# Optimization experiments

Hardware: AMD Instinct MI355X
Metric: run time of the kernel (lower is better)

The kernel has to match this reference:

```python
import jax, jax.numpy as jnp
import numpy as np

K_N = 20          # neighbors (init kwarg k_n)
EPS = 1e-5        # BN / InstanceNorm eps (torch default)


def _conv1x1(x, w, b):
    # x: [B,C,N,K], w: [O,C], b: [O]
    return jnp.einsum('bcnk,oc->bonk', x, w) + b[None, :, None, None]


def _bn(x, g, b):
    # training-mode BatchNorm2d: stats over (B,N,K)
    mean = x.mean(axis=(0, 2, 3), keepdims=True)
    var = x.var(axis=(0, 2, 3), keepdims=True)
    return (x - mean) * jax.lax.rsqrt(var + EPS) * g[None, :, None, None] + b[None, :, None, None]


def _inorm(x):
    # InstanceNorm2d (affine=False): stats over (N,K) per (b,c)
    mean = x.mean(axis=(2, 3), keepdims=True)
    var = x.var(axis=(2, 3), keepdims=True)
    return (x - mean) * jax.lax.rsqrt(var + EPS)


def _knn(x, k):
    # x: [B,C,N] -> idx [B,N,k] of nearest neighbors (excluding self)
    sq = jnp.sum(x * x, axis=1)                                   # [B,N]
    neg_d = 2.0 * jnp.einsum('bcn,bcm->bnm', x, x) - sq[:, :, None] - sq[:, None, :]
    _, idx = jax.lax.top_k(neg_d, k + 1)
    return idx[:, :, 1:]


def _res_block(x, w1, b1, g1, be1, w2, b2, g2, be2):
    # pre=False: residual branch is identity
    out = jax.nn.relu(_bn(_inorm(_conv1x1(x, w1, b1)), g1, be1))
    out = _bn(_inorm(_conv1x1(out, w2, b2)), g2, be2)
    return jax.nn.relu(out + x)


def _forward(data, conv0_w, conv0_b, bn0_g, bn0_b, lin_w, lin_b,
             res_w1, res_b1, res_g1, res_be1, res_w2, res_b2, res_g2, res_be2):
    B, C, N = data.shape
    # graph_feature: degree feature from normalized affinity matrix
    nrm = jnp.linalg.norm(data, axis=1, keepdims=True) + 1e-5
    o = data / nrm
    A = jnp.einsum('bcn,bcm->bnm', o, o)                          # [B,N,N]
    D = (jnp.sum(A, axis=1, keepdims=True) - 1.0) / N             # [B,1,N] (subtract eye diag)
    feat = jnp.concatenate([data, jax.nn.relu(jnp.tanh(D))], axis=1)  # [B,129,N]

    idx = _knn(feat, K_N)                                         # [B,N,k]
    xt = jnp.transpose(feat, (0, 2, 1))                           # [B,N,129]
    gathered = jax.vmap(lambda xb, ib: xb[ib])(xt, idx)           # [B,N,k,129]
    center = xt[:, :, None, :]
    edge = jnp.concatenate([jnp.broadcast_to(center, gathered.shape),
                            center - gathered], axis=3)           # [B,N,k,258]
    edge = jnp.transpose(edge, (0, 3, 1, 2))                      # [B,258,N,k]

    out = jax.nn.relu(_bn(_conv1x1(edge, conv0_w, conv0_b), bn0_g, bn0_b))
    out = jnp.max(out, axis=3, keepdims=True)                     # max_pool2d (1,k) -> [B,128,N,1]
    for i in range(4):
        out = _res_block(out, res_w1[i], res_b1[i], res_g1[i], res_be1[i],
                         res_w2[i], res_b2[i], res_g2[i], res_be2[i])
    logit = _conv1x1(out, lin_w, lin_b)                           # [B,1,N,1]
    return logit.reshape(logit.shape[0], -1)                      # [B,N]


def setup_inputs() -> dict:
    B, C, N = 8, 128, 2048
    key = jax.random.key(0)
    ks = jax.random.split(key, 10)
    s = 0.05
    return {
        'data': jax.random.normal(ks[0], (B, C, N), dtype=jnp.float32),
        'x': jax.random.normal(ks[1], (B, C, N), dtype=jnp.float32),  # unused by module
        'conv0_w': jax.random.normal(ks[2], (128, 258), dtype=jnp.float32) * s,
        'conv0_b': jnp.zeros((128,), dtype=jnp.float32),
        'bn0_g': jnp.ones((128,), dtype=jnp.float32),
        'bn0_b': jnp.zeros((128,), dtype=jnp.float32),
        'lin_w': jax.random.normal(ks[3], (1, 128), dtype=jnp.float32) * s,
        'lin_b': jnp.zeros((1,), dtype=jnp.float32),
        'res_w1': jax.random.normal(ks[4], (4, 128, 128), dtype=jnp.float32) * s,
        'res_b1': jnp.zeros((4, 128), dtype=jnp.float32),
        'res_g1': jnp.ones((4, 128), dtype=jnp.float32),
        'res_be1': jnp.zeros((4, 128), dtype=jnp.float32),
        'res_w2': jax.random.normal(ks[5], (4, 128, 128), dtype=jnp.float32) * s,
        'res_b2': jnp.zeros((4, 128), dtype=jnp.float32),
        'res_g2': jnp.ones((4, 128), dtype=jnp.float32),
        'res_be2': jnp.zeros((4, 128), dtype=jnp.float32),
    }


def reference(data, x, conv0_w, conv0_b, bn0_g, bn0_b, lin_w, lin_b,
              res_w1, res_b1, res_g1, res_be1, res_w2, res_b2, res_g2, res_be2):
    # x is accepted but unused, matching the torch module
    return _forward(data, conv0_w, conv0_b, bn0_g, bn0_b, lin_w, lin_b,
                    res_w1, res_b1, res_g1, res_be1, res_w2, res_b2, res_g2, res_be2)
```

## Files before the change

kernel.cpp:

```cpp
#include <hip/hip_runtime.h>
#include <math.h>
#include <float.h>

#define NB 8
#define NC 128
#define NN 2048
#define KNN 20
#define EPSV 1e-5f

#define S_OFF      0
#define BN0S_OFF   1024
#define RESST_OFF  1280
#define ZERO_CNT   17664
#define NRM_OFF    17664
#define SQN_OFF    34048
#define F1_OFF     50432
#define WCAT_OFF   66816
#define WCOL_OFF   99584
#define F128_OFF   99840
#define PQ_OFF     2463232
#define X_OFF      6657536
#define SLOT_SZ    2097152
#define IDX_OFF    12948992
#define G_OFF      13276672
#define XB_OFF     46831104
#define WS_FLOATS  48928256
#define MMN_OFF    (X_OFF + SLOT_SZ)
#define MMX_OFF    (X_OFF + 2 * SLOT_SZ)

__launch_bounds__(256)
__global__ void k1_fused(const float* __restrict__ data, float* __restrict__ ws) {
    int b = blockIdx.y;
    int n0 = blockIdx.x * 64;
    int tid = threadIdx.x;
    __shared__ float tile[128][65];
    __shared__ float red[4][64];
    __shared__ float Linv[64];
    int g = tid >> 6, nn = tid & 63;
    const float* dp = data + (size_t)b * NC * NN + n0 + nn;
    float sq = 0.f;
    for (int c = g; c < 128; c += 4) {
        float v = dp[(size_t)c * NN];
        tile[c][nn] = v;
        sq = fmaf(v, v, sq);
    }
    red[g][nn] = sq;
    __syncthreads();
    if (tid < 64) {
        float s = red[0][tid] + red[1][tid] + red[2][tid] + red[3][tid];
        ws[NRM_OFF + b * NN + n0 + tid] = s;
        Linv[tid] = 1.f / (sqrtf(s) + 1e-5f);
    }
    __syncthreads();
    if (tid < 128) {
        float s = 0.f;
#pragma unroll 8
        for (int j = 0; j < 64; ++j) s = fmaf(tile[tid][j], Linv[j], s);
        atomicAdd(&ws[S_OFF + b * NC + tid], s);
    }
}

__launch_bounds__(256)
__global__ void k2_feat(const float* __restrict__ data, float* __restrict__ ws) {
    int b = blockIdx.y;
    int n0 = blockIdx.x * 64;
    int tid = threadIdx.x;
    __shared__ float Sb[NC];
    __shared__ float fT[64][129];
    __shared__ float redD[4][64];
    if (tid < NC) Sb[tid] = ws[S_OFF + b * NC + tid];
    __syncthreads();
    int nn = tid & 63, cg = tid >> 6;
    float dotp = 0.f;
    const float* dp = data + (size_t)b * NC * NN + n0 + nn;
    for (int c = cg; c < NC; c += 4) {
        float v = dp[(size_t)c * NN];
        fT[nn][c] = v;
        dotp = fmaf(Sb[c], v, dotp);
    }
    redD[cg][nn] = dotp;
    __syncthreads();
    if (tid < 64) {
        float dt = redD[0][tid] + redD[1][tid] + redD[2][tid] + redD[3][tid];
        float nrmsq = ws[NRM_OFF + b * NN + n0 + tid];
        float nrm = sqrtf(nrmsq) + 1e-5f;
        float D = (dt / nrm - 1.f) * (1.f / (float)NN);
        float f1 = tanhf(D); if (f1 < 0.f) f1 = 0.f;
        ws[F1_OFF + b * NN + n0 + tid] = f1;
        ws[SQN_OFF + b * NN + n0 + tid] = nrmsq + f1 * f1;
    }
    __syncthreads();
    float* out = ws + F128_OFF + (size_t)(b * NN + n0) * 128;
    for (int i = tid; i < 64 * 128; i += 256) out[i] = fT[i >> 7][i & 127];
}

__launch_bounds__(256)
__global__ void k4_wcat(const float* __restrict__ w, float* __restrict__ ws) {
    int i = blockIdx.x * 256 + threadIdx.x;
    if (i < 32768) {
        int o = i >> 7, c = i & 127;
        float v = (o < 128) ? w[o * 258 + c] + w[o * 258 + 129 + c]
                            : w[(o - 128) * 258 + 129 + c];
        ws[WCAT_OFF + i] = v;
    } else if (i < 33024) {
        int o = i - 32768;
        float v = (o < 128) ? w[o * 258 + 128] + w[o * 258 + 257]
                            : w[(o - 128) * 258 + 257];
        ws[WCOL_OFF + o] = v;
    }
}

__launch_bounds__(256)
__global__ void k3_gram(float* __restrict__ ws) {
    __shared__ __align__(16) float As[8][64];
    __shared__ __align__(16) float Bs[8][128];
    int tid = threadIdx.x;
    int b = blockIdx.z;
    int p = blockIdx.x >> 1, half = blockIdx.x & 1;
    int a = 0, rem = 16;
    while (p >= rem) { p -= rem; ++a; --rem; }
    int bq = a + p;
    int n0 = a * 128 + half * 64, m0 = bq * 128;
    const float* F = ws + F128_OFF + (size_t)b * NN * 128;
    float acc[4][8];
#pragma unroll
    for (int i = 0; i < 4; ++i)
#pragma unroll
        for (int j = 0; j < 8; ++j) acc[i][j] = 0.f;
    int rr = tid >> 1, cq = tid & 1;
    int ar = (tid & 127) >> 1, acq = tid & 1;
    int tx = tid & 15, ty = tid >> 4;
    for (int kc = 0; kc < 128; kc += 8) {
        float4 bv = *(const float4*)&F[(size_t)(m0 + rr) * 128 + kc + cq * 4];
        float4 av;
        if (tid < 128) av = *(const float4*)&F[(size_t)(n0 + ar) * 128 + kc + acq * 4];
        __syncthreads();
        Bs[cq*4+0][rr] = bv.x; Bs[cq*4+1][rr] = bv.y; Bs[cq*4+2][rr] = bv.z; Bs[cq*4+3][rr] = bv.w;
        if (tid < 128) {
            As[acq*4+0][ar] = av.x; As[acq*4+1][ar] = av.y;
            As[acq*4+2][ar] = av.z; As[acq*4+3][ar] = av.w;
        }
        __syncthreads();
#pragma unroll
        for (int kk = 0; kk < 8; ++kk) {
            float aa[4], bb[8];
            *(float4*)&aa[0] = *(const float4*)&As[kk][ty * 4];
            *(float4*)&bb[0] = *(const float4*)&Bs[kk][tx * 4];
            *(float4*)&bb[4] = *(const float4*)&Bs[kk][64 + tx * 4];
#pragma unroll
            for (int i = 0; i < 4; ++i)
#pragma unroll
                for (int j = 0; j < 8; ++j) acc[i][j] = fmaf(aa[i], bb[j], acc[i][j]);
        }
    }
    const float* F1 = ws + F1_OFF + b * NN;
    const float* SQ = ws + SQN_OFF + b * NN;
    float sqv[8], f1m[8], sqn[4], f1nv[4];
#pragma unroll
    for (int j = 0; j < 4; ++j) {
        sqv[j]     = SQ[m0 + tx * 4 + j];
        sqv[4 + j] = SQ[m0 + 64 + tx * 4 + j];
        f1m[j]     = F1[m0 + tx * 4 + j];
        f1m[4 + j] = F1[m0 + 64 + tx * 4 + j];
    }
#pragma unroll
    for (int i = 0; i < 4; ++i) {
        int n = n0 + ty * 4 + i;
        sqn[i]  = SQ[n];
        f1nv[i] = F1[n];
    }
    float* G = ws + G_OFF + (size_t)b * NN * NN;
#pragma unroll
    for (int i = 0; i < 4; ++i) {
        int row = n0 + ty * 4 + i;
        float f1n = f1nv[i];
        float4 o1, o2;
        o1.x = 2.f*fmaf(f1n, f1m[0], acc[i][0]) - sqv[0];
        o1.y = 2.f*fmaf(f1n, f1m[1], acc[i][1]) - sqv[1];
        o1.z = 2.f*fmaf(f1n, f1m[2], acc[i][2]) - sqv[2];
        o1.w = 2.f*fmaf(f1n, f1m[3], acc[i][3]) - sqv[3];
        o2.x = 2.f*fmaf(f1n, f1m[4], acc[i][4]) - sqv[4];
        o2.y = 2.f*fmaf(f1n, f1m[5], acc[i][5]) - sqv[5];
        o2.z = 2.f*fmaf(f1n, f1m[6], acc[i][6]) - sqv[6];
        o2.w = 2.f*fmaf(f1n, f1m[7], acc[i][7]) - sqv[7];
        *(float4*)&G[(size_t)row * NN + m0 + tx * 4]      = o1;
        *(float4*)&G[(size_t)row * NN + m0 + 64 + tx * 4] = o2;
    }
    if (a != bq) {
#pragma unroll
        for (int j = 0; j < 8; ++j) {
            int cl = (j < 4) ? (tx * 4 + j) : (64 + tx * 4 + (j - 4));
            size_t grow = (size_t)(m0 + cl) * NN + n0 + ty * 4;
            float f1mj = f1m[j];
            float4 t0;
            t0.x = 2.f*fmaf(f1nv[0], f1mj, acc[0][j]) - sqn[0];
            t0.y = 2.f*fmaf(f1nv[1], f1mj, acc[1][j]) - sqn[1];
            t0.z = 2.f*fmaf(f1nv[2], f1mj, acc[2][j]) - sqn[2];
            t0.w = 2.f*fmaf(f1nv[3], f1mj, acc[3][j]) - sqn[3];
            *(float4*)&G[grow] = t0;
        }
    }
}

__launch_bounds__(256)
__global__ void ksel(float* __restrict__ ws) {
    int wid = threadIdx.x >> 6, lane = threadIdx.x & 63;
    int r = blockIdx.x * 4 + wid;
    const float* row = ws + G_OFF + (size_t)r * NN;
    float v[32];
#pragma unroll
    for (int i = 0; i < 8; ++i)
        *(float4*)&v[i * 4] = *(const float4*)&row[lane * 32 + i * 4];
    float b1v = -FLT_MAX, b2v = -FLT_MAX;
    int b1i = 0, b2i = 0;
#pragma unroll
    for (int i = 0; i < 32; ++i) {
        float x = v[i];
        if (x > b1v)      { b2v = b1v; b2i = b1i; b1v = x; b1i = i; }
        else if (x > b2v) { b2v = x; b2i = i; }
    }
    unsigned int mask = 0u;
    bool has2 = true;
    int* out = (int*)(ws + IDX_OFF) + (size_t)r * KNN;
    for (int k = 0; k < 21; ++k) {
        float M = b1v;
#pragma unroll
        for (int off = 1; off < 64; off <<= 1) M = fmaxf(M, __shfl_xor(M, off));
        unsigned long long tied = __ballot(b1v == M);
        int mm;
        if (__popcll(tied) > 1) {
            int cand = (b1v == M) ? ((lane << 5) | b1i) : 0x7FFFFFFF;
#pragma unroll
            for (int off = 1; off < 64; off <<= 1) {
                int oc = __shfl_xor(cand, off);
                cand = oc < cand ? oc : cand;
            }
            mm = cand;
        } else {
            int l = __ffsll(tied) - 1;
            mm = (l << 5) | __shfl(b1i, l);
        }
        if (k > 0 && lane == 0) out[k - 1] = mm;
        if (lane == (mm >> 5)) {
            mask |= 1u << b1i;
            if (has2) { b1v = b2v; b1i = b2i; has2 = false; }
            else {
                b1v = -FLT_MAX; b2v = -FLT_MAX; b1i = 0; b2i = 0;
#pragma unroll
                for (int i = 0; i < 32; ++i) {
                    float x = (mask & (1u << i)) ? -FLT_MAX : v[i];
                    if (x > b1v)      { b2v = b1v; b2i = b1i; b1v = x; b1i = i; }
                    else if (x > b2v) { b2v = x; b2i = i; }
                }
                has2 = true;
            }
        }
    }
}

__launch_bounds__(256)
__global__ void k5_pq(float* __restrict__ ws) {
    __shared__ __align__(16) float As[16][64];
    __shared__ __align__(16) float Bs[16][64];
    int tid = threadIdx.x;
    int m0 = blockIdx.x * 64, o0 = blockIdx.y * 64;
    int rr = tid >> 2, cq = tid & 3;
    int tx = tid & 15, ty = tid >> 4;
    float acc[4][4];
#pragma unroll
    for (int i = 0; i < 4; ++i)
#pragma unroll
        for (int j = 0; j < 4; ++j) acc[i][j] = 0.f;
    const float* F  = ws + F128_OFF;
    const float* Wc = ws + WCAT_OFF;
    for (int kc = 0; kc < 128; kc += 16) {
        float4 av = *(const float4*)&F [(size_t)(m0 + rr) * 128 + kc + cq * 4];
        float4 bv = *(const float4*)&Wc[(size_t)(o0 + rr) * 128 + kc + cq * 4];
        __syncthreads();
        As[cq*4+0][rr]=av.x; As[cq*4+1][rr]=av.y; As[cq*4+2][rr]=av.z; As[cq*4+3][rr]=av.w;
        Bs[cq*4+0][rr]=bv.x; Bs[cq*4+1][rr]=bv.y; Bs[cq*4+2][rr]=bv.z; Bs[cq*4+3][rr]=bv.w;
        __syncthreads();
#pragma unroll
        for (int kk = 0; kk < 16; ++kk) {
            float a[4], bb[4];
            *(float4*)&a[0]  = *(const float4*)&As[kk][ty * 4];
            *(float4*)&bb[0] = *(const float4*)&Bs[kk][tx * 4];
#pragma unroll
            for (int i = 0; i < 4; ++i)
#pragma unroll
                for (int j = 0; j < 4; ++j) acc[i][j] = fmaf(a[i], bb[j], acc[i][j]);
        }
    }
    float wc[4], f1v[4];
#pragma unroll
    for (int j = 0; j < 4; ++j) {
        wc[j]  = ws[WCOL_OFF + o0 + tx * 4 + j];
        f1v[j] = ws[F1_OFF + m0 + ty * 4 + j];
    }
#pragma unroll
    for (int i = 0; i < 4; ++i) {
        float4 o;
        o.x = fmaf(f1v[i], wc[0], acc[i][0]);
        o.y = fmaf(f1v[i], wc[1], acc[i][1]);
        o.z = fmaf(f1v[i], wc[2], acc[i][2]);
        o.w = fmaf(f1v[i], wc[3], acc[i][3]);
        *(float4*)&ws[PQ_OFF + (size_t)(m0 + ty * 4 + i) * 256 + o0 + tx * 4] = o;
    }
}

__launch_bounds__(256)
__global__ void k6_bn0stats(float* __restrict__ ws) {
    int tid = threadIdx.x;
    int o = tid & 127, h = tid >> 7;
    int m0 = blockIdx.x * 16;
    const float* PQ = ws + PQ_OFF;
    const int* idx = (const int*)(ws + IDX_OFF);
    float* MMn = ws + MMN_OFF;
    float* MMx = ws + MMX_OFF;
    __shared__ float red[2][128];
    float s = 0.f, q = 0.f;
    for (int p = h; p < 16; p += 2) {
        int m = m0 + p;
        int bb = m >> 11;
        float pv = PQ[(size_t)m * 256 + o];
        const int* ip = idx + (size_t)m * KNN;
        float mn = FLT_MAX, mx = -FLT_MAX;
        for (int k = 0; k < KNN; ++k) {
            int j = ip[k];
            float val = pv - PQ[(size_t)(bb * NN + j) * 256 + 128 + o];
            s += val; q += val * val;
            mn = fminf(mn, val); mx = fmaxf(mx, val);
        }
        MMn[(size_t)m * NC + o] = mn;
        MMx[(size_t)m * NC + o] = mx;
    }
    red[h][o] = s; __syncthreads();
    if (tid < 128) atomicAdd(&ws[BN0S_OFF + tid], red[0][tid] + red[1][tid]);
    __syncthreads();
    red[h][o] = q; __syncthreads();
    if (tid < 128) atomicAdd(&ws[BN0S_OFF + 128 + tid], red[0][tid] + red[1][tid]);
}

__launch_bounds__(256)
__global__ void k8_apply(float* __restrict__ ws, const float* __restrict__ g,
                         const float* __restrict__ be) {
    int e = blockIdx.x * 256 + threadIdx.x;
    int fi = e * 4;
    int o = fi & 127;
    const float cnt = 1.f / (float)(NB * NN * KNN);
    float4 sum4 = *(const float4*)&ws[BN0S_OFF + o];
    float4 ssq4 = *(const float4*)&ws[BN0S_OFF + 128 + o];
    float4 g4   = *(const float4*)&g[o];
    float4 be4  = *(const float4*)&be[o];
    float4 mn = *(const float4*)&ws[MMN_OFF + fi];
    float4 mx = *(const float4*)&ws[MMX_OFF + fi];
    float4 r;
#define BN0_DO(comp) { \
    float m_ = sum4.comp * cnt; \
    float v_ = ssq4.comp * cnt - m_ * m_; if (v_ < 0.f) v_ = 0.f; \
    float sc_ = g4.comp * rsqrtf(v_ + EPSV); \
    float sh_ = be4.comp - m_ * sc_; \
    r.comp = fmaxf(fmaf(sc_ > 0.f ? mx.comp : mn.comp, sc_, sh_), 0.f); }
    BN0_DO(x) BN0_DO(y) BN0_DO(z) BN0_DO(w)
#undef BN0_DO
    *(float4*)&ws[X_OFF + fi] = r;
}

__launch_bounds__(256)
__global__ void k9f_conv(const float* __restrict__ x, const float* __restrict__ w,
                         float* __restrict__ y, float* __restrict__ stats,
                         const float* __restrict__ statsIn,
                         const float* __restrict__ g, const float* __restrict__ be,
                         const float* __restrict__ xin, float* __restrict__ xw) {
    __shared__ __align__(16) float As[16][64];
    __shared__ __align__(16) float Bs[16][64];
    __shared__ float red[16][64];
    __shared__ float vvv[8][128];
    __shared__ float scs[128], shs[128];
    int tid = threadIdx.x;
    int m0 = blockIdx.x * 64, o0 = blockIdx.y * 64;
    int bA = m0 >> 11;
    if (statsIn) {
        for (int e = tid; e < 1024; e += 256) {
            float sum = statsIn[e], ssq = statsIn[1024 + e];
            float m_ = sum * (1.f / (float)NN);
            float v_ = ssq * (1.f / (float)NN) - m_ * m_; if (v_ < 0.f) v_ = 0.f;
            vvv[e >> 7][e & 127] = v_ / (v_ + EPSV);
        }
        __syncthreads();
        if (tid < 128) {
            float a = 0.f;
#pragma unroll
            for (int b2 = 0; b2 < NB; ++b2) a += vvv[b2][tid];
            float rsbn = rsqrtf(a * (1.f / (float)NB) + EPSV);
            float sum = statsIn[bA * 128 + tid], ssq = statsIn[1024 + bA * 128 + tid];
            float m_ = sum * (1.f / (float)NN);
            float v_ = ssq * (1.f / (float)NN) - m_ * m_; if (v_ < 0.f) v_ = 0.f;
            float sc_ = rsqrtf(v_ + EPSV) * rsbn * g[tid];
            scs[tid] = sc_;
            shs[tid] = be[tid] - m_ * sc_;
        }
        __syncthreads();
    }
    int rr = tid >> 2, cq = tid & 3;
    int tx = tid & 15, ty = tid >> 4;
    float acc[4][4];
#pragma unroll
    for (int i = 0; i < 4; ++i)
#pragma unroll
        for (int j = 0; j < 4; ++j) acc[i][j] = 0.f;
    for (int kc = 0; kc < NC; kc += 16) {
        float4 av = *(const float4*)&x[(size_t)(m0 + rr) * NC + kc + cq * 4];
        if (statsIn) {
            int c = kc + cq * 4;
            av.x = fmaf(av.x, scs[c],     shs[c]);
            av.y = fmaf(av.y, scs[c + 1], shs[c + 1]);
            av.z = fmaf(av.z, scs[c + 2], shs[c + 2]);
            av.w = fmaf(av.w, scs[c + 3], shs[c + 3]);
            if (xin) {
                float4 xv = *(const float4*)&xin[(size_t)(m0 + rr) * NC + kc + cq * 4];
                av.x += xv.x; av.y += xv.y; av.z += xv.z; av.w += xv.w;
            }
            av.x = fmaxf(av.x, 0.f); av.y = fmaxf(av.y, 0.f);
            av.z = fmaxf(av.z, 0.f); av.w = fmaxf(av.w, 0.f);
            if (xw && blockIdx.y == 0)
                *(float4*)&xw[(size_t)(m0 + rr) * NC + kc + cq * 4] = av;
        }
        float4 bv = *(const float4*)&w[(size_t)(o0 + rr) * NC + kc + cq * 4];
        __syncthreads();
        As[cq*4+0][rr]=av.x; As[cq*4+1][rr]=av.y; As[cq*4+2][rr]=av.z; As[cq*4+3][rr]=av.w;
        Bs[cq*4+0][rr]=bv.x; Bs[cq*4+1][rr]=bv.y; Bs[cq*4+2][rr]=bv.z; Bs[cq*4+3][rr]=bv.w;
        __syncthreads();
#pragma unroll
        for (int kk = 0; kk < 16; ++kk) {
            float a[4], bb[4];
            *(float4*)&a[0]  = *(const float4*)&As[kk][ty * 4];
            *(float4*)&bb[0] = *(const float4*)&Bs[kk][tx * 4];
#pragma unroll
            for (int i = 0; i < 4; ++i)
#pragma unroll
                for (int j = 0; j < 4; ++j) acc[i][j] = fmaf(a[i], bb[j], acc[i][j]);
        }
    }
#pragma unroll
    for (int i = 0; i < 4; ++i) {
        float4 o;
        o.x = acc[i][0]; o.y = acc[i][1]; o.z = acc[i][2]; o.w = acc[i][3];
        *(float4*)&y[(size_t)(m0 + ty * 4 + i) * NC + o0 + tx * 4] = o;
    }
    float s[4], q[4];
#pragma unroll
    for (int j = 0; j < 4; ++j) {
        s[j] = acc[0][j] + acc[1][j] + acc[2][j] + acc[3][j];
        q[j] = acc[0][j]*acc[0][j] + acc[1][j]*acc[1][j] + acc[2][j]*acc[2][j] + acc[3][j]*acc[3][j];
    }
    *(float4*)&red[ty][tx * 4] = make_float4(s[0], s[1], s[2], s[3]);
    __syncthreads();
    if (tid < 64) {
        float t = 0.f;
#pragma unroll
        for (int g2 = 0; g2 < 16; ++g2) t += red[g2][tid];
        atomicAdd(&stats[bA * NC + o0 + tid], t);
    }
    __syncthreads();
    *(float4*)&red[ty][tx * 4] = make_float4(q[0], q[1], q[2], q[3]);
    __syncthreads();
    if (tid < 64) {
        float t = 0.f;
#pragma unroll
        for (int g2 = 0; g2 < 16; ++g2) t += red[g2][tid];
        atomicAdd(&stats[1024 + bA * NC + o0 + tid], t);
    }
}

__launch_bounds__(256)
__global__ void k12_logit(const float* __restrict__ y2, const float* __restrict__ xin,
                          const float* __restrict__ statsIn,
                          const float* __restrict__ g, const float* __restrict__ be,
                          const float* __restrict__ lw, const float* __restrict__ lb,
                          float* __restrict__ out) {
    __shared__ float wsh[128];
    __shared__ float vvv[8][128];
    __shared__ float scs[128], shs[128];
    int tid = threadIdx.x;
    int b = (blockIdx.x * 256) >> 11;
    if (tid < 128) wsh[tid] = lw[tid];
    for (int e = tid; e < 1024; e += 256) {
        float sum = statsIn[e], ssq = statsIn[1024 + e];
        float m_ = sum * (1.f / (float)NN);
        float v_ = ssq * (1.f / (float)NN) - m_ * m_; if (v_ < 0.f) v_ = 0.f;
        vvv[e >> 7][e & 127] = v_ / (v_ + EPSV);
    }
    __syncthreads();
    if (tid < 128) {
        float a = 0.f;
#pragma unroll
        for (int b2 = 0; b2 < NB; ++b2) a += vvv[b2][tid];
        float rsbn = rsqrtf(a * (1.f / (float)NB) + EPSV);
        float sum = statsIn[b * 128 + tid], ssq = statsIn[1024 + b * 128 + tid];
        float m_ = sum * (1.f / (float)NN);
        float v_ = ssq * (1.f / (float)NN) - m_ * m_; if (v_ < 0.f) v_ = 0.f;
        float sc_ = rsqrtf(v_ + EPSV) * rsbn * g[tid];
        scs[tid] = sc_;
        shs[tid] = be[tid] - m_ * sc_;
    }
    __syncthreads();
    int m = blockIdx.x * 256 + tid;
    const float* yp = y2 + (size_t)m * NC;
    const float* xp = xin + (size_t)m * NC;
    float acc = lb[0];
    for (int c = 0; c < NC; c += 4) {
        float4 yv = *(const float4*)&yp[c];
        float4 xv = *(const float4*)&xp[c];
        float v0 = fmaxf(fmaf(yv.x, scs[c],     shs[c])     + xv.x, 0.f);
        float v1 = fmaxf(fmaf(yv.y, scs[c + 1], shs[c + 1]) + xv.y, 0.f);
        float v2 = fmaxf(fmaf(yv.z, scs[c + 2], shs[c + 2]) + xv.z, 0.f);
        float v3 = fmaxf(fmaf(yv.w, scs[c + 3], shs[c + 3]) + xv.w, 0.f);
        acc += v0 * wsh[c] + v1 * wsh[c + 1] + v2 * wsh[c + 2] + v3 * wsh[c + 3];
    }
    out[m] = acc;
}

extern "C" void kernel_launch(void* const* d_in, const int* in_sizes, int n_in,
                              void* d_out, int out_size, void* d_ws, size_t ws_size,
                              hipStream_t stream) {
    if (ws_size < (size_t)WS_FLOATS * 4) return;
    const float* data    = (const float*)d_in[0];
    const float* conv0_w = (const float*)d_in[2];
    const float* bn0_g   = (const float*)d_in[4];
    const float* bn0_b   = (const float*)d_in[5];
    const float* lin_w   = (const float*)d_in[6];
    const float* lin_b   = (const float*)d_in[7];
    const float* res_w1  = (const float*)d_in[8];
    const float* res_g1  = (const float*)d_in[10];
    const float* res_be1 = (const float*)d_in[11];
    const float* res_w2  = (const float*)d_in[12];
    const float* res_g2  = (const float*)d_in[14];
    const float* res_be2 = (const float*)d_in[15];
    float* ws  = (float*)d_ws;
    float* out = (float*)d_out;

    hipMemsetAsync(d_ws, 0, ZERO_CNT * sizeof(float), stream);
    k1_fused<<<dim3(32, 8), 256, 0, stream>>>(data, ws);
    k2_feat<<<dim3(32, 8), 256, 0, stream>>>(data, ws);
    k4_wcat<<<130, 256, 0, stream>>>(conv0_w, ws);
    k3_gram<<<dim3(272, 1, 8), 256, 0, stream>>>(ws);
    ksel<<<4096, 256, 0, stream>>>(ws);
    k5_pq<<<dim3(256, 4), 256, 0, stream>>>(ws);
    k6_bn0stats<<<1024, 256, 0, stream>>>(ws);
    k8_apply<<<2048, 256, 0, stream>>>(ws, bn0_g, bn0_b);

    float* XA = ws + X_OFF;
    float* Y1 = ws + X_OFF + SLOT_SZ;
    float* Y2 = ws + X_OFF + 2 * SLOT_SZ;
    float* XB = ws + XB_OFF;
    float* ST = ws + RESST_OFF;

    k9f_conv<<<dim3(256, 2), 256, 0, stream>>>(XA, res_w1, Y1, ST,
                                               nullptr, nullptr, nullptr, nullptr, nullptr);
    k9f_conv<<<dim3(256, 2), 256, 0, stream>>>(Y1, res_w2, Y2, ST + 2048,
                                               ST, res_g1, res_be1, nullptr, nullptr);
    float* xcur = XA; float* xnext = XB;
    for (int i = 1; i < 4; ++i) {
        int L = 2 * i, L2 = 2 * i + 1;
        k9f_conv<<<dim3(256, 2), 256, 0, stream>>>(Y2, res_w1 + i * 16384, Y1, ST + L * 2048,
                                                   ST + (L - 1) * 2048,
                                                   res_g2 + (i - 1) * 128, res_be2 + (i - 1) * 128,
                                                   xcur, xnext);
        k9f_conv<<<dim3(256, 2), 256, 0, stream>>>(Y1, res_w2 + i * 16384, Y2, ST + L2 * 2048,
                                                   ST + L * 2048,
                                                   res_g1 + i * 128, res_be1 + i * 128,
                                                   nullptr, nullptr);
        float* t = xcur; xcur = xnext; xnext = t;
    }
    k12_logit<<<64, 256, 0, stream>>>(Y2, xcur, ST + 7 * 2048, res_g2 + 3 * 128, res_be2 + 3 * 128,
                                      lin_w, lin_b, out);
}
```

Before: 372.6 us.

## Shrink gram and conv tiles, and coalesce row loads in top-k selection

The Gram kernel now uses 32-row tiles instead of 64, and the residual 1x1 conv kernel uses 32-row tiles with 2x4 per-thread accumulators instead of 4x4, which doubles the grid sizes. The aim is more blocks in flight on the many compute units, at the cost of less reuse per loaded B tile and more global traffic. The selection kernel now loads each row interleaved (lane*4 + i*256) so the float4 reads are coalesced, and it remaps local-to-global column indices, tie-breaking and ownership checks to match.

```diff
diff --git a/kernel.cpp b/kernel.cpp
--- a/kernel.cpp
+++ b/kernel.cpp
@@ -112,50 +112,51 @@
 
 __launch_bounds__(256)
 __global__ void k3_gram(float* __restrict__ ws) {
-    __shared__ __align__(16) float As[8][64];
+    __shared__ __align__(16) float As[8][32];
     __shared__ __align__(16) float Bs[8][128];
     int tid = threadIdx.x;
     int b = blockIdx.z;
-    int p = blockIdx.x >> 1, half = blockIdx.x & 1;
+    int p = blockIdx.x >> 2, quarter = blockIdx.x & 3;
     int a = 0, rem = 16;
     while (p >= rem) { p -= rem; ++a; --rem; }
     int bq = a + p;
-    int n0 = a * 128 + half * 64, m0 = bq * 128;
+    int n0 = a * 128 + quarter * 32, m0 = bq * 128;
     const float* F = ws + F128_OFF + (size_t)b * NN * 128;
-    float acc[4][8];
-#pragma unroll
-    for (int i = 0; i < 4; ++i)
+    float acc[2][8];
+#pragma unroll
+    for (int i = 0; i < 2; ++i)
 #pragma unroll
         for (int j = 0; j < 8; ++j) acc[i][j] = 0.f;
     int rr = tid >> 1, cq = tid & 1;
-    int ar = (tid & 127) >> 1, acq = tid & 1;
+    int ar = (tid & 63) >> 1, acq = tid & 1;
     int tx = tid & 15, ty = tid >> 4;
     for (int kc = 0; kc < 128; kc += 8) {
         float4 bv = *(const float4*)&F[(size_t)(m0 + rr) * 128 + kc + cq * 4];
         float4 av;
-        if (tid < 128) av = *(const float4*)&F[(size_t)(n0 + ar) * 128 + kc + acq * 4];
+        if (tid < 64) av = *(const float4*)&F[(size_t)(n0 + ar) * 128 + kc + acq * 4];
         __syncthreads();
         Bs[cq*4+0][rr] = bv.x; Bs[cq*4+1][rr] = bv.y; Bs[cq*4+2][rr] = bv.z; Bs[cq*4+3][rr] = bv.w;
-        if (tid < 128) {
+        if (tid < 64) {
             As[acq*4+0][ar] = av.x; As[acq*4+1][ar] = av.y;
             As[acq*4+2][ar] = av.z; As[acq*4+3][ar] = av.w;
         }
         __syncthreads();
 #pragma unroll
         for (int kk = 0; kk < 8; ++kk) {
-            float aa[4], bb[8];
-            *(float4*)&aa[0] = *(const float4*)&As[kk][ty * 4];
+            float a0 = As[kk][ty * 2], a1 = As[kk][ty * 2 + 1];
+            float bb[8];
             *(float4*)&bb[0] = *(const float4*)&Bs[kk][tx * 4];
             *(float4*)&bb[4] = *(const float4*)&Bs[kk][64 + tx * 4];
 #pragma unroll
-            for (int i = 0; i < 4; ++i)
-#pragma unroll
-                for (int j = 0; j < 8; ++j) acc[i][j] = fmaf(aa[i], bb[j], acc[i][j]);
+            for (int j = 0; j < 8; ++j) {
+                acc[0][j] = fmaf(a0, bb[j], acc[0][j]);
+                acc[1][j] = fmaf(a1, bb[j], acc[1][j]);
+            }
         }
     }
     const float* F1 = ws + F1_OFF + b * NN;
     const float* SQ = ws + SQN_OFF + b * NN;
-    float sqv[8], f1m[8], sqn[4], f1nv[4];
+    float sqv[8], f1m[8], sqn[2], f1nv[2];
 #pragma unroll
     for (int j = 0; j < 4; ++j) {
         sqv[j]     = SQ[m0 + tx * 4 + j];
@@ -164,15 +165,15 @@
         f1m[4 + j] = F1[m0 + 64 + tx * 4 + j];
     }
 #pragma unroll
-    for (int i = 0; i < 4; ++i) {
-        int n = n0 + ty * 4 + i;
+    for (int i = 0; i < 2; ++i) {
+        int n = n0 + ty * 2 + i;
         sqn[i]  = SQ[n];
         f1nv[i] = F1[n];
     }
     float* G = ws + G_OFF + (size_t)b * NN * NN;
 #pragma unroll
-    for (int i = 0; i < 4; ++i) {
-        int row = n0 + ty * 4 + i;
+    for (int i = 0; i < 2; ++i) {
+        int row = n0 + ty * 2 + i;
         float f1n = f1nv[i];
         float4 o1, o2;
         o1.x = 2.f*fmaf(f1n, f1m[0], acc[i][0]) - sqv[0];
@@ -190,14 +191,12 @@
 #pragma unroll
         for (int j = 0; j < 8; ++j) {
             int cl = (j < 4) ? (tx * 4 + j) : (64 + tx * 4 + (j - 4));
-            size_t grow = (size_t)(m0 + cl) * NN + n0 + ty * 4;
+            size_t grow = (size_t)(m0 + cl) * NN + n0 + ty * 2;
             float f1mj = f1m[j];
-            float4 t0;
+            float2 t0;
             t0.x = 2.f*fmaf(f1nv[0], f1mj, acc[0][j]) - sqn[0];
             t0.y = 2.f*fmaf(f1nv[1], f1mj, acc[1][j]) - sqn[1];
-            t0.z = 2.f*fmaf(f1nv[2], f1mj, acc[2][j]) - sqn[2];
-            t0.w = 2.f*fmaf(f1nv[3], f1mj, acc[3][j]) - sqn[3];
-            *(float4*)&G[grow] = t0;
+            *(float2*)&G[grow] = t0;
         }
     }
 }
@@ -210,7 +209,7 @@
     float v[32];
 #pragma unroll
     for (int i = 0; i < 8; ++i)
-        *(float4*)&v[i * 4] = *(const float4*)&row[lane * 32 + i * 4];
+        *(float4*)&v[i * 4] = *(const float4*)&row[i * 256 + lane * 4];
     float b1v = -FLT_MAX, b2v = -FLT_MAX;
     int b1i = 0, b2i = 0;
 #pragma unroll
@@ -229,7 +228,7 @@
         unsigned long long tied = __ballot(b1v == M);
         int mm;
         if (__popcll(tied) > 1) {
-            int cand = (b1v == M) ? ((lane << 5) | b1i) : 0x7FFFFFFF;
+            int cand = (b1v == M) ? ((b1i >> 2) * 256 + lane * 4 + (b1i & 3)) : 0x7FFFFFFF;
 #pragma unroll
             for (int off = 1; off < 64; off <<= 1) {
                 int oc = __shfl_xor(cand, off);
@@ -238,21 +237,26 @@
             mm = cand;
         } else {
             int l = __ffsll(tied) - 1;
-            mm = (l << 5) | __shfl(b1i, l);
+            int s = __shfl(b1i, l);
+            mm = (s >> 2) * 256 + l * 4 + (s & 3);
         }
         if (k > 0 && lane == 0) out[k - 1] = mm;
-        if (lane == (mm >> 5)) {
-            mask |= 1u << b1i;
-            if (has2) { b1v = b2v; b1i = b2i; has2 = false; }
-            else {
-                b1v = -FLT_MAX; b2v = -FLT_MAX; b1i = 0; b2i = 0;
-#pragma unroll
-                for (int i = 0; i < 32; ++i) {
-                    float x = (mask & (1u << i)) ? -FLT_MAX : v[i];
-                    if (x > b1v)      { b2v = b1v; b2i = b1i; b1v = x; b1i = i; }
-                    else if (x > b2v) { b2v = x; b2i = i; }
+        if (lane == ((mm & 255) >> 2)) {
+            int s_mine = b1i;
+            int col_mine = (s_mine >> 2) * 256 + lane * 4 + (s_mine & 3);
+            if (col_mine == mm) {
+                mask |= 1u << b1i;
+                if (has2) { b1v = b2v; b1i = b2i; has2 = false; }
+                else {
+                    b1v = -FLT_MAX; b2v = -FLT_MAX; b1i = 0; b2i = 0;
+#pragma unroll
+                    for (int i = 0; i < 32; ++i) {
+                        float x = (mask & (1u << i)) ? -FLT_MAX : v[i];
+                        if (x > b1v)      { b2v = b1v; b2i = b1i; b1v = x; b1i = i; }
+                        else if (x > b2v) { b2v = x; b2i = i; }
+                    }
+                    has2 = true;
                 }
-                has2 = true;
             }
         }
     }
@@ -372,13 +376,13 @@
                          const float* __restrict__ statsIn,
                          const float* __restrict__ g, const float* __restrict__ be,
                          const float* __restrict__ xin, float* __restrict__ xw) {
-    __shared__ __align__(16) float As[16][64];
+    __shared__ __align__(16) float As[16][32];
     __shared__ __align__(16) float Bs[16][64];
     __shared__ float red[16][64];
     __shared__ float vvv[8][128];
     __shared__ float scs[128], shs[128];
     int tid = threadIdx.x;
-    int m0 = blockIdx.x * 64, o0 = blockIdx.y * 64;
+    int m0 = blockIdx.x * 32, o0 = blockIdx.y * 64;
     int bA = m0 >> 11;
     if (statsIn) {
         for (int e = tid; e < 1024; e += 256) {
@@ -403,56 +407,64 @@
         __syncthreads();
     }
     int rr = tid >> 2, cq = tid & 3;
+    int ar = (tid & 127) >> 2, acq = tid & 3;
     int tx = tid & 15, ty = tid >> 4;
-    float acc[4][4];
-#pragma unroll
-    for (int i = 0; i < 4; ++i)
+    float acc[2][4];
+#pragma unroll
+    for (int i = 0; i < 2; ++i)
 #pragma unroll
         for (int j = 0; j < 4; ++j) acc[i][j] = 0.f;
     for (int kc = 0; kc < NC; kc += 16) {
-        float4 av = *(const float4*)&x[(size_t)(m0 + rr) * NC + kc + cq * 4];
-        if (statsIn) {
-            int c = kc + cq * 4;
-            av.x = fmaf(av.x, scs[c],     shs[c]);
-            av.y = fmaf(av.y, scs[c + 1], shs[c + 1]);
-            av.z = fmaf(av.z, scs[c + 2], shs[c + 2]);
-            av.w = fmaf(av.w, scs[c + 3], shs[c + 3]);
-            if (xin) {
-                float4 xv = *(const float4*)&xin[(size_t)(m0 + rr) * NC + kc + cq * 4];
-                av.x += xv.x; av.y += xv.y; av.z += xv.z; av.w += xv.w;
+        float4 av;
+        if (tid < 128) {
+            av = *(const float4*)&x[(size_t)(m0 + ar) * NC + kc + acq * 4];
+            if (statsIn) {
+                int c = kc + acq * 4;
+                av.x = fmaf(av.x, scs[c],     shs[c]);
+                av.y = fmaf(av.y, scs[c + 1], shs[c + 1]);
+                av.z = fmaf(av.z, scs[c + 2], shs[c + 2]);
+                av.w = fmaf(av.w, scs[c + 3], shs[c + 3]);
+                if (xin) {
+                    float4 xv = *(const float4*)&xin[(size_t)(m0 + ar) * NC + kc + acq * 4];
+                    av.x += xv.x; av.y += xv.y; av.z += xv.z; av.w += xv.w;
+                }
+                av.x = fmaxf(av.x, 0.f); av.y = fmaxf(av.y, 0.f);
+                av.z = fmaxf(av.z, 0.f); av.w = fmaxf(av.w, 0.f);
+                if (xw && blockIdx.y == 0)
+                    *(float4*)&xw[(size_t)(m0 + ar) * NC + kc + acq * 4] = av;
             }
-            av.x = fmaxf(av.x, 0.f); av.y = fmaxf(av.y, 0.f);
-            av.z = fmaxf(av.z, 0.f); av.w = fmaxf(av.w, 0.f);
-            if (xw && blockIdx.y == 0)
-                *(float4*)&xw[(size_t)(m0 + rr) * NC + kc + cq * 4] = av;
         }
         float4 bv = *(const float4*)&w[(size_t)(o0 + rr) * NC + kc + cq * 4];
         __syncthreads();
-        As[cq*4+0][rr]=av.x; As[cq*4+1][rr]=av.y; As[cq*4+2][rr]=av.z; As[cq*4+3][rr]=av.w;
+        if (tid < 128) {
+            As[acq*4+0][ar]=av.x; As[acq*4+1][ar]=av.y;
+            As[acq*4+2][ar]=av.z; As[acq*4+3][ar]=av.w;
+        }
         Bs[cq*4+0][rr]=bv.x; Bs[cq*4+1][rr]=bv.y; Bs[cq*4+2][rr]=bv.z; Bs[cq*4+3][rr]=bv.w;
         __syncthreads();
 #pragma unroll
         for (int kk = 0; kk < 16; ++kk) {
-            float a[4], bb[4];
-            *(float4*)&a[0]  = *(const float4*)&As[kk][ty * 4];
+            float a0 = As[kk][ty * 2], a1 = As[kk][ty * 2 + 1];
+            float bb[4];
             *(float4*)&bb[0] = *(const float4*)&Bs[kk][tx * 4];
 #pragma unroll
-            for (int i = 0; i < 4; ++i)
-#pragma unroll
-                for (int j = 0; j < 4; ++j) acc[i][j] = fmaf(a[i], bb[j], acc[i][j]);
-        }
-    }
-#pragma unroll
-    for (int i = 0; i < 4; ++i) {
+            for (int j = 0; j < 4; ++j) {
+                acc[0][j] = fmaf(a0, bb[j], acc[0][j]);
+                acc[1][j] = fmaf(a1, bb[j], acc[1][j]);
+            }
+        }
+    }
+#pragma unroll
+    for (int i = 0; i < 2; ++i) {
         float4 o;
         o.x = acc[i][0]; o.y = acc[i][1]; o.z = acc[i][2]; o.w = acc[i][3];
-        *(float4*)&y[(size_t)(m0 + ty * 4 + i) * NC + o0 + tx * 4] = o;
+        *(float4*)&y[(size_t)(m0 + ty * 2 + i) * NC + o0 + tx * 4] = o;
     }
     float s[4], q[4];
 #pragma unroll
     for (int j = 0; j < 4; ++j) {
-        s[j] = acc[0][j] + acc[1][j] + acc[2][j] + acc[3][j];
-        q[j] = acc[0][j]*acc[0][j] + acc[1][j]*acc[1][j] + acc[2][j]*acc[2][j] + acc[3][j]*acc[3][j];
+        s[j] = acc[0][j] + acc[1][j];
+        q[j] = acc[0][j]*acc[0][j] + acc[1][j]*acc[1][j];
     }
     *(float4*)&red[ty][tx * 4] = make_float4(s[0], s[1], s[2], s[3]);
     __syncthreads();
@@ -544,7 +556,7 @@
     k1_fused<<<dim3(32, 8), 256, 0, stream>>>(data, ws);
     k2_feat<<<dim3(32, 8), 256, 0, stream>>>(data, ws);
     k4_wcat<<<130, 256, 0, stream>>>(conv0_w, ws);
-    k3_gram<<<dim3(272, 1, 8), 256, 0, stream>>>(ws);
+    k3_gram<<<dim3(544, 1, 8), 256, 0, stream>>>(ws);
     ksel<<<4096, 256, 0, stream>>>(ws);
     k5_pq<<<dim3(256, 4), 256, 0, stream>>>(ws);
     k6_bn0stats<<<1024, 256, 0, stream>>>(ws);
@@ -556,18 +568,18 @@
     float* XB = ws + XB_OFF;
     float* ST = ws + RESST_OFF;
 
-    k9f_conv<<<dim3(256, 2), 256, 0, stream>>>(XA, res_w1, Y1, ST,
+    k9f_conv<<<dim3(512, 2), 256, 0, stream>>>(XA, res_w1, Y1, ST,
                                                nullptr, nullptr, nullptr, nullptr, nullptr);
-    k9f_conv<<<dim3(256, 2), 256, 0, stream>>>(Y1, res_w2, Y2, ST + 2048,
+    k9f_conv<<<dim3(512, 2), 256, 0, stream>>>(Y1, res_w2, Y2, ST + 2048,
                                                ST, res_g1, res_be1, nullptr, nullptr);
     float* xcur = XA; float* xnext = XB;
     for (int i = 1; i < 4; ++i) {
         int L = 2 * i, L2 = 2 * i + 1;
-        k9f_conv<<<dim3(256, 2), 256, 0, stream>>>(Y2, res_w1 + i * 16384, Y1, ST + L * 2048,
+        k9f_conv<<<dim3(512, 2), 256, 0, stream>>>(Y2, res_w1 + i * 16384, Y1, ST + L * 2048,
                                                    ST + (L - 1) * 2048,
                                                    res_g2 + (i - 1) * 128, res_be2 + (i - 1) * 128,
                                                    xcur, xnext);
-        k9f_conv<<<dim3(256, 2), 256, 0, stream>>>(Y1, res_w2 + i * 16384, Y2, ST + L2 * 2048,
+        k9f_conv<<<dim3(512, 2), 256, 0, stream>>>(Y1, res_w2 + i * 16384, Y2, ST + L2 * 2048,
                                                    ST + L * 2048,
                                                    res_g1 + i * 128, res_be1 + i * 128,
                                                    nullptr, nullptr);
```

New measurement: 417.2 us. +12.0%, slower.
